# Kernel optimization log

Measured on AMD Instinct MI355X. Metric: run time of the kernel, lower is better.

## Reference

```python
import jax, jax.numpy as jnp
import numpy as np

N = 50000   # nodes
E = 625000  # edges
H = 128     # hidden
B = 32      # bottleneck_dim


def _layernorm(x, g, b, eps=1e-5):
    m = jnp.mean(x, axis=-1, keepdims=True)
    v = jnp.var(x, axis=-1, keepdims=True)
    return (x - m) * jax.lax.rsqrt(v + eps) * g + b


def setup_inputs() -> dict:
    key = jax.random.key(0)
    ks = jax.random.split(key, 16)
    s = 0.05
    return {
        "x": jax.random.normal(ks[0], (N, H), dtype=jnp.float32),
        "edge_index": jax.random.randint(ks[1], (2, E), 0, N, dtype=jnp.int64),
        # down GINConv (eps trainable, init 0) + its bottleneck MLP
        "eps_down": jnp.zeros((), jnp.float32),
        "dw1": jax.random.normal(ks[2], (H, B), dtype=jnp.float32) * s,
        "dg1": jnp.ones((B,), jnp.float32),
        "db1": jnp.zeros((B,), jnp.float32),
        "dw2": jax.random.normal(ks[3], (B, H), dtype=jnp.float32) * s,
        # up GINConv
        "eps_up": jnp.zeros((), jnp.float32),
        "uw1": jax.random.normal(ks[4], (H, B), dtype=jnp.float32) * s,
        "ug1": jnp.ones((B,), jnp.float32),
        "ub1": jnp.zeros((B,), jnp.float32),
        "uw2": jax.random.normal(ks[5], (B, H), dtype=jnp.float32) * s,
        # outer LayerNorms
        "ln1_g": jnp.ones((H,), jnp.float32),
        "ln1_b": jnp.zeros((H,), jnp.float32),
        "ln2_g": jnp.ones((H,), jnp.float32),
        "ln2_b": jnp.zeros((H,), jnp.float32),
        # direction embeddings [2, H]
        "dir_emb": jax.random.normal(ks[6], (2, H), dtype=jnp.float32) * 0.02,
        # combine Linear(2H -> H) with bias
        "cw": jax.random.normal(ks[7], (2 * H, H), dtype=jnp.float32) * s,
        "cb": jnp.zeros((H,), jnp.float32),
    }


def reference(x, edge_index, eps_down, dw1, dg1, db1, dw2,
              eps_up, uw1, ug1, ub1, uw2,
              ln1_g, ln1_b, ln2_g, ln2_b, dir_emb, cw, cb):
    src, dst = edge_index[0], edge_index[1]

    def gin(s_idx, d_idx, eps, w1, g1, b1, w2):
        # scatter-add of source features onto destination nodes
        agg = jax.ops.segment_sum(x[s_idx], d_idx, num_segments=N)  # [N, H]
        h = (1.0 + eps) * x + agg
        # bottleneck MLP: Linear -> LayerNorm -> ReLU -> (Dropout=id) -> Linear
        h = _layernorm(h @ w1, g1, b1)
        return jax.nn.relu(h) @ w2  # [N, H]

    h_down = _layernorm(jax.nn.relu(gin(src, dst, eps_down, dw1, dg1, db1, dw2) + dir_emb[0]), ln1_g, ln1_b)
    # reversed edges for the "up" direction
    h_up = _layernorm(jax.nn.relu(gin(dst, src, eps_up, uw1, ug1, ub1, uw2) + dir_emb[1]), ln2_g, ln2_b)

    h_cat = jnp.concatenate([h_down, h_up], axis=-1)  # [N, 2H]
    return h_cat @ cw + cb  # [N, H]
```

## Files before the change

kernel.cpp:

```cpp
#include <hip/hip_runtime.h>

#define N_NODES 50000
#define NPAD 50048
#define N_EDGES 625000
#define H 128
#define B 32
#define PSTRIDE 40
#define CAP 64
#define NPART 8
#define ROWS_PER_PART (2 * N_NODES / NPART)
#define NGRP 3125
#define YGB 1564
#define CVB 160
#define FILLB (2443 * NPART)

using bf16x8  = __attribute__((ext_vector_type(8))) short;
using f32x4   = __attribute__((ext_vector_type(4))) float;
using u16x4   = __attribute__((ext_vector_type(4))) unsigned short;

static __device__ __forceinline__ unsigned short f2bf(float f) {
    unsigned u = __float_as_uint(f);
    unsigned r = (u + 0x7fff + ((u >> 16) & 1)) >> 16;
    return (unsigned short)r;
}
static __device__ __forceinline__ float bf2f(unsigned short h) {
    return __uint_as_float(((unsigned)h) << 16);
}

__global__ __launch_bounds__(256) void front_kernel(
    const int* __restrict__ ei, int* __restrict__ cursor,
    unsigned short* __restrict__ bucket,
    const float* __restrict__ x,
    const float* __restrict__ dw1, const float* __restrict__ uw1,
    const float* __restrict__ dw2, const float* __restrict__ uw2,
    const float* __restrict__ cw,
    unsigned short* __restrict__ w2h, unsigned short* __restrict__ w2l,
    unsigned short* __restrict__ cwh,
    unsigned short* __restrict__ y)
{
    __shared__ unsigned short wh_lds[32 * 136];
    __shared__ unsigned short wl_lds[32 * 136];

    int b = blockIdx.x;
    if (b < YGB) {
        int dir = (b >= 782) ? 1 : 0;
        int r0b = (b - dir * 782) * 64;
        const float* w1src = dir ? uw1 : dw1;
        for (int j = threadIdx.x; j < 4096; j += 256) {
            int k = j >> 5, c = j & 31;
            float v = w1src[j];
            unsigned short h = f2bf(v);
            wh_lds[c * 136 + k] = h;
            wl_lds[c * 136 + k] = f2bf(v - bf2f(h));
        }
        __syncthreads();

        int w = threadIdx.x >> 6, lane = threadIdx.x & 63;
        int l15 = lane & 15, g = lane >> 4;
        int r0 = r0b + w * 16;
        int node = r0 + l15; if (node >= N_NODES) node = N_NODES - 1;
        const float* xrow = x + (size_t)node * H;

        f32x4 acc[2];
        acc[0] = (f32x4){0.f,0.f,0.f,0.f};
        acc[1] = (f32x4){0.f,0.f,0.f,0.f};
        #pragma unroll
        for (int ks = 0; ks < 4; ++ks) {
            int ko = ks * 32 + g * 8;
            float4 xa = *(const float4*)(xrow + ko);
            float4 xc = *(const float4*)(xrow + ko + 4);
            union { bf16x8 v; unsigned short u[8]; } bb;
            bb.u[0] = f2bf(xa.x); bb.u[1] = f2bf(xa.y);
            bb.u[2] = f2bf(xa.z); bb.u[3] = f2bf(xa.w);
            bb.u[4] = f2bf(xc.x); bb.u[5] = f2bf(xc.y);
            bb.u[6] = f2bf(xc.z); bb.u[7] = f2bf(xc.w);
            #pragma unroll
            for (int t = 0; t < 2; ++t) {
                bf16x8 ah = *(const bf16x8*)(wh_lds + (t * 16 + l15) * 136 + ko);
                bf16x8 al = *(const bf16x8*)(wl_lds + (t * 16 + l15) * 136 + ko);
                acc[t] = __builtin_amdgcn_mfma_f32_16x16x32_bf16(ah, bb.v, acc[t], 0, 0, 0);
                acc[t] = __builtin_amdgcn_mfma_f32_16x16x32_bf16(al, bb.v, acc[t], 0, 0, 0);
            }
        }

        unsigned short* orow = y + ((size_t)dir * NPAD + r0 + l15) * B;
        #pragma unroll
        for (int t = 0; t < 2; ++t) {
            u16x4 o = {f2bf(acc[t][0]), f2bf(acc[t][1]), f2bf(acc[t][2]), f2bf(acc[t][3])};
            *(u16x4*)(orow + t * 16 + g * 4) = o;
        }
        return;
    }
    if (b < YGB + CVB) {
        int i = (b - YGB) * 256 + threadIdx.x;
        if (i < 8192) {
            int j = i & 4095;
            int c = j >> 5, k = j & 31;
            const float* src = (i >> 12) ? uw2 : dw2;
            float v = src[k * 128 + c];
            unsigned short h = f2bf(v);
            w2h[i] = h; w2l[i] = f2bf(v - bf2f(h));
        } else {
            int j = i - 8192;
            int c = j >> 8, k = j & 255;
            cwh[j] = f2bf(cw[k * 128 + c]);
        }
        return;
    }
    int fb = b - (YGB + CVB);
    int p  = fb & 7;
    int eb = fb >> 3;
    int e = eb * 256 + threadIdx.x;
    if (e >= N_EDGES) return;
    int lo = p * ROWS_PER_PART, hi = lo + ROWS_PER_PART;
    int s = ei[e];
    int d = ei[N_EDGES + e];
    int r2 = N_NODES + s;
    if (d >= lo && d < hi) {
        int pos = atomicAdd(&cursor[d], 1);
        if (pos < CAP)
            __builtin_nontemporal_store((unsigned short)s, bucket + (size_t)d * CAP + pos);
    }
    if (r2 >= lo && r2 < hi) {
        int pos = atomicAdd(&cursor[r2], 1);
        if (pos < CAP)
            __builtin_nontemporal_store((unsigned short)d, bucket + (size_t)r2 * CAP + pos);
    }
}

__global__ __launch_bounds__(256) void gather_mlp_kernel(
    const unsigned* __restrict__ y,
    const int* __restrict__ cursor, const unsigned short* __restrict__ bucket,
    const float* __restrict__ eps_d_p, const float* __restrict__ eps_u_p,
    const unsigned short* __restrict__ w2bT_hi, const unsigned short* __restrict__ w2bT_lo,
    const float* __restrict__ dg1, const float* __restrict__ db1,
    const float* __restrict__ ug1, const float* __restrict__ ub1,
    const float* __restrict__ ln1g, const float* __restrict__ ln1b,
    const float* __restrict__ ln2g, const float* __restrict__ ln2b,
    const float* __restrict__ dir_emb,
    unsigned short* __restrict__ hcat)
{
    __shared__ unsigned short plds[4][2][16 * PSTRIDE];

    int w = threadIdx.x >> 6, lane = threadIdx.x & 63;
    int sgrp = lane >> 4, l16 = lane & 15;
    int blk = blockIdx.x;
    int dir = (blk >= 782) ? 1 : 0;
    int r0 = (blk - dir * 782) * 64 + w * 16;

    float eps = 1.f + (dir ? eps_u_p[0] : eps_d_p[0]);
    const unsigned* yu = y + (size_t)dir * NPAD * 16;

    const float* g1p = dir ? ug1 : dg1;
    const float* b1p = dir ? ub1 : db1;
    float2 gv = ((const float2*)g1p)[l16];
    float2 bv = ((const float2*)b1p)[l16];

    unsigned short* mh = &plds[w][0][0];
    unsigned short* ml = &plds[w][1][0];

    for (int p = 0; p < 4; ++p) {
        int rloc = p * 4 + sgrp;
        int node = r0 + rloc;
        float p0 = 0.f, p1 = 0.f;
        if (node < N_NODES) {
            int ridx = dir * N_NODES + node;
            int deg = cursor[ridx]; if (deg > CAP) deg = CAP;
            const unsigned short* nb = bucket + (size_t)ridx * CAP;
            float a0 = 0.f, a1 = 0.f;
            for (int base = 0; base < deg; base += 16) {
                int m = deg - base; if (m > 16) m = 16;
                int id = (l16 < m) ? (int)nb[base + l16] : 0;
                int lim = m - 1;
                for (int j = 0; j < m; j += 8) {
                    unsigned r[8];
                    #pragma unroll
                    for (int q = 0; q < 8; ++q) {
                        int idx = j + q; if (idx > lim) idx = lim;
                        int nbid = __shfl(id, (sgrp << 4) + idx);
                        r[q] = yu[nbid * 16 + l16];
                    }
                    #pragma unroll
                    for (int q = 0; q < 8; ++q) {
                        if (j + q <= lim) {
                            a0 += __uint_as_float(r[q] << 16);
                            a1 += __uint_as_float(r[q] & 0xffff0000u);
                        }
                    }
                }
            }
            unsigned sv = yu[node * 16 + l16];
            float c0 = eps * __uint_as_float(sv << 16) + a0;
            float c1 = eps * __uint_as_float(sv & 0xffff0000u) + a1;
            float ss = c0 + c1, s2 = c0 * c0 + c1 * c1;
            #pragma unroll
            for (int m2 = 1; m2 <= 8; m2 <<= 1) {
                ss += __shfl_xor(ss, m2);
                s2 += __shfl_xor(s2, m2);
            }
            float mean = ss * (1.f / 32.f);
            float var  = s2 * (1.f / 32.f) - mean * mean;
            float rs   = rsqrtf(var + 1e-5f);
            p0 = fmaxf((c0 - mean) * rs * gv.x + bv.x, 0.f);
            p1 = fmaxf((c1 - mean) * rs * gv.y + bv.y, 0.f);
        }
        unsigned short q0 = f2bf(p0), q1 = f2bf(p1);
        *(unsigned*)(mh + rloc * PSTRIDE + 2 * l16) = ((unsigned)q1 << 16) | q0;
        *(unsigned*)(ml + rloc * PSTRIDE + 2 * l16) =
            ((unsigned)f2bf(p1 - bf2f(q1)) << 16) | f2bf(p0 - bf2f(q0));
    }

    int l15 = lane & 15, g = lane >> 4;

    const unsigned short* w2h = w2bT_hi + dir * 4096;
    const unsigned short* w2l = w2bT_lo + dir * 4096;

    bf16x8 pbh = *(const bf16x8*)(mh + l15 * PSTRIDE + g * 8);
    bf16x8 pbl = *(const bf16x8*)(ml + l15 * PSTRIDE + g * 8);

    f32x4 acc2[8];
    #pragma unroll
    for (int t = 0; t < 8; ++t) acc2[t] = (f32x4){0.f,0.f,0.f,0.f};
    #pragma unroll
    for (int t = 0; t < 8; ++t) {
        bf16x8 ah = *(const bf16x8*)(w2h + (t * 16 + l15) * 32 + g * 8);
        bf16x8 al = *(const bf16x8*)(w2l + (t * 16 + l15) * 32 + g * 8);
        acc2[t] = __builtin_amdgcn_mfma_f32_16x16x32_bf16(ah, pbh, acc2[t], 0, 0, 0);
        acc2[t] = __builtin_amdgcn_mfma_f32_16x16x32_bf16(al, pbh, acc2[t], 0, 0, 0);
        acc2[t] = __builtin_amdgcn_mfma_f32_16x16x32_bf16(ah, pbl, acc2[t], 0, 0, 0);
    }

    float av[8][4];
    float u = 0.f, u2 = 0.f;
    #pragma unroll
    for (int t = 0; t < 8; ++t) {
        float4 de = *(const float4*)(dir_emb + dir * H + t * 16 + g * 4);
        av[t][0] = fmaxf(acc2[t][0] + de.x, 0.f);
        av[t][1] = fmaxf(acc2[t][1] + de.y, 0.f);
        av[t][2] = fmaxf(acc2[t][2] + de.z, 0.f);
        av[t][3] = fmaxf(acc2[t][3] + de.w, 0.f);
        #pragma unroll
        for (int r = 0; r < 4; ++r) { u += av[t][r]; u2 += av[t][r] * av[t][r]; }
    }
    u  += __shfl_xor(u, 16);  u  += __shfl_xor(u, 32);
    u2 += __shfl_xor(u2, 16); u2 += __shfl_xor(u2, 32);
    float m2  = u * (1.f / 128.f);
    float v2  = u2 * (1.f / 128.f) - m2 * m2;
    float rs2 = rsqrtf(v2 + 1e-5f);

    const float* lgp = dir ? ln2g : ln1g;
    const float* lbp = dir ? ln2b : ln1b;
    if ((r0 + l15) < N_NODES) {
        unsigned short* orow = hcat + (size_t)(r0 + l15) * 256 + dir * 128;
        #pragma unroll
        for (int t = 0; t < 8; ++t) {
            float4 gg = *(const float4*)(lgp + t * 16 + g * 4);
            float4 bb = *(const float4*)(lbp + t * 16 + g * 4);
            u16x4 o;
            o[0] = f2bf((av[t][0] - m2) * rs2 * gg.x + bb.x);
            o[1] = f2bf((av[t][1] - m2) * rs2 * gg.y + bb.y);
            o[2] = f2bf((av[t][2] - m2) * rs2 * gg.z + bb.z);
            o[3] = f2bf((av[t][3] - m2) * rs2 * gg.w + bb.w);
            *(u16x4*)(orow + t * 16 + g * 4) = o;
        }
    }
}

__global__ __launch_bounds__(256) void combine_mfma(
    const unsigned short* __restrict__ hcat,
    const unsigned short* __restrict__ cwh,
    const float* __restrict__ cb, float* __restrict__ out)
{
    int w = threadIdx.x >> 6, lane = threadIdx.x & 63;
    int l15 = lane & 15, g = lane >> 4;
    int gid = blockIdx.x * 4 + w;
    int q = gid & 3;
    int j = gid >> 2;

    const unsigned short* abase = cwh + (size_t)(q * 32 + l15) * 256 + g * 8;
    bf16x8 Ah[2][8];
    #pragma unroll
    for (int t = 0; t < 2; ++t)
        #pragma unroll
        for (int ks = 0; ks < 8; ++ks)
            Ah[t][ks] = *(const bf16x8*)(abase + (t * 16) * 256 + ks * 32);

    int grp[4]; int ng = 0;
    #pragma unroll
    for (int k = 0; k < 4; ++k) {
        int gg = j + 782 * k;
        if (gg < NGRP) grp[ng++] = gg;
    }
    if (ng == 0) return;

    bf16x8 Bc[8], Bn[8];
    {
        const unsigned short* bb = hcat + (size_t)grp[0] * 16 * 256 + l15 * 256 + g * 8;
        #pragma unroll
        for (int ks = 0; ks < 8; ++ks) Bc[ks] = *(const bf16x8*)(bb + ks * 32);
    }

    float4 bias0 = *(const float4*)(cb + q * 32 + g * 4);
    float4 bias1 = *(const float4*)(cb + q * 32 + 16 + g * 4);

    for (int i = 0; i < ng; ++i) {
        if (i + 1 < ng) {
            const unsigned short* bb = hcat + (size_t)grp[i + 1] * 16 * 256 + l15 * 256 + g * 8;
            #pragma unroll
            for (int ks = 0; ks < 8; ++ks) Bn[ks] = *(const bf16x8*)(bb + ks * 32);
        }

        f32x4 acc0 = (f32x4){0.f,0.f,0.f,0.f};
        f32x4 acc1 = (f32x4){0.f,0.f,0.f,0.f};
        #pragma unroll
        for (int ks = 0; ks < 8; ++ks) {
            acc0 = __builtin_amdgcn_mfma_f32_16x16x32_bf16(Ah[0][ks], Bc[ks], acc0, 0, 0, 0);
            acc1 = __builtin_amdgcn_mfma_f32_16x16x32_bf16(Ah[1][ks], Bc[ks], acc1, 0, 0, 0);
        }

        float* orow = out + (size_t)(grp[i] * 16 + l15) * 128 + q * 32;
        f32x4 v0 = acc0, v1 = acc1;
        v0[0] += bias0.x; v0[1] += bias0.y; v0[2] += bias0.z; v0[3] += bias0.w;
        v1[0] += bias1.x; v1[1] += bias1.y; v1[2] += bias1.z; v1[3] += bias1.w;
        *(f32x4*)(orow + g * 4) = v0;
        *(f32x4*)(orow + 16 + g * 4) = v1;

        #pragma unroll
        for (int ks = 0; ks < 8; ++ks) Bc[ks] = Bn[ks];
    }
}

extern "C" void kernel_launch(void* const* d_in, const int* in_sizes, int n_in,
                              void* d_out, int out_size, void* d_ws, size_t ws_size,
                              hipStream_t stream) {
    const float* x     = (const float*)d_in[0];
    const int*   ei    = (const int*)d_in[1];
    const float* eps_d = (const float*)d_in[2];
    const float* dw1   = (const float*)d_in[3];
    const float* dg1   = (const float*)d_in[4];
    const float* db1   = (const float*)d_in[5];
    const float* dw2   = (const float*)d_in[6];
    const float* eps_u = (const float*)d_in[7];
    const float* uw1   = (const float*)d_in[8];
    const float* ug1   = (const float*)d_in[9];
    const float* ub1   = (const float*)d_in[10];
    const float* uw2   = (const float*)d_in[11];
    const float* ln1g  = (const float*)d_in[12];
    const float* ln1b  = (const float*)d_in[13];
    const float* ln2g  = (const float*)d_in[14];
    const float* ln2b  = (const float*)d_in[15];
    const float* dire  = (const float*)d_in[16];
    const float* cw    = (const float*)d_in[17];
    const float* cb    = (const float*)d_in[18];

    int* cursor = (int*)d_ws;
    unsigned short* bucket = (unsigned short*)(cursor + 2 * N_NODES);
    unsigned short* yarr = bucket + (size_t)2 * N_NODES * CAP;
    unsigned short* hcat = yarr + (size_t)2 * NPAD * B;
    unsigned short* w2bT_hi = hcat + (size_t)N_NODES * 256;
    unsigned short* w2bT_lo = w2bT_hi + 8192;
    unsigned short* cwbT_hi = w2bT_lo + 8192;

    hipMemsetAsync(cursor, 0, 2 * N_NODES * sizeof(int), stream);

    front_kernel<<<YGB + CVB + FILLB, 256, 0, stream>>>(
        ei, cursor, bucket, x, dw1, uw1, dw2, uw2, cw,
        w2bT_hi, w2bT_lo, cwbT_hi, yarr);

    gather_mlp_kernel<<<1564, 256, 0, stream>>>(
        (const unsigned*)yarr, cursor, bucket, eps_d, eps_u,
        w2bT_hi, w2bT_lo,
        dg1, db1, ug1, ub1, ln1g, ln1b, ln2g, ln2b, dire, hcat);

    combine_mfma<<<782, 256, 0, stream>>>(hcat, cwbT_hi, cb, (float*)d_out);
}
```

Baseline: 145.8 us.

## Replace per-partition edge fill with two-pass LDS binning and staged scatter

The old edge fill read the edge list once per partition, launching eight blocks per edge chunk. Each block appended to a partition's bucket only when the destination fell inside it. Now each block reads its edges once and bins packed (row, neighbour) entries by partition in LDS. It flushes each bin to a contiguous per-partition staging region with one global atomic per bin. A new scatter kernel then walks each partition's staging region and does the per-row atomic bucket inserts, so the atomics are localized per partition. This cuts redundant edge reads but adds a kernel launch and a round trip through a roughly 5.9 MB staging buffer.

```diff
diff --git a/kernel.cpp b/kernel.cpp
--- a/kernel.cpp
+++ b/kernel.cpp
@@ -12,7 +12,10 @@
 #define NGRP 3125
 #define YGB 1564
 #define CVB 160
-#define FILLB (2443 * NPART)
+#define EPB 1024
+#define BINB ((N_EDGES + EPB - 1) / EPB)
+#define NS 512
+#define SLOT 184320
 
 using bf16x8  = __attribute__((ext_vector_type(8))) short;
 using f32x4   = __attribute__((ext_vector_type(4))) float;
@@ -28,8 +31,9 @@
 }
 
 __global__ __launch_bounds__(256) void front_kernel(
-    const int* __restrict__ ei, int* __restrict__ cursor,
-    unsigned short* __restrict__ bucket,
+    const int* __restrict__ ei, int* __restrict__ bin_cursor,
+    int* __restrict__ cursor, unsigned short* __restrict__ bucket,
+    unsigned* __restrict__ staging,
     const float* __restrict__ x,
     const float* __restrict__ dw1, const float* __restrict__ uw1,
     const float* __restrict__ dw2, const float* __restrict__ uw2,
@@ -38,8 +42,10 @@
     unsigned short* __restrict__ cwh,
     unsigned short* __restrict__ y)
 {
-    __shared__ unsigned short wh_lds[32 * 136];
-    __shared__ unsigned short wl_lds[32 * 136];
+    __shared__ union {
+        struct { unsigned short wh[32 * 136], wl[32 * 136]; } yg;
+        struct { unsigned bins[NPART][NS]; int bcnt[NPART]; } bn;
+    } sm;
 
     int b = blockIdx.x;
     if (b < YGB) {
@@ -50,8 +56,8 @@
             int k = j >> 5, c = j & 31;
             float v = w1src[j];
             unsigned short h = f2bf(v);
-            wh_lds[c * 136 + k] = h;
-            wl_lds[c * 136 + k] = f2bf(v - bf2f(h));
+            sm.yg.wh[c * 136 + k] = h;
+            sm.yg.wl[c * 136 + k] = f2bf(v - bf2f(h));
         }
         __syncthreads();
 
@@ -76,8 +82,8 @@
             bb.u[6] = f2bf(xc.z); bb.u[7] = f2bf(xc.w);
             #pragma unroll
             for (int t = 0; t < 2; ++t) {
-                bf16x8 ah = *(const bf16x8*)(wh_lds + (t * 16 + l15) * 136 + ko);
-                bf16x8 al = *(const bf16x8*)(wl_lds + (t * 16 + l15) * 136 + ko);
+                bf16x8 ah = *(const bf16x8*)(sm.yg.wh + (t * 16 + l15) * 136 + ko);
+                bf16x8 al = *(const bf16x8*)(sm.yg.wl + (t * 16 + l15) * 136 + ko);
                 acc[t] = __builtin_amdgcn_mfma_f32_16x16x32_bf16(ah, bb.v, acc[t], 0, 0, 0);
                 acc[t] = __builtin_amdgcn_mfma_f32_16x16x32_bf16(al, bb.v, acc[t], 0, 0, 0);
             }
@@ -107,24 +113,73 @@
         }
         return;
     }
+    if (threadIdx.x < NPART) sm.bn.bcnt[threadIdx.x] = 0;
+    __syncthreads();
+
     int fb = b - (YGB + CVB);
-    int p  = fb & 7;
-    int eb = fb >> 3;
-    int e = eb * 256 + threadIdx.x;
-    if (e >= N_EDGES) return;
-    int lo = p * ROWS_PER_PART, hi = lo + ROWS_PER_PART;
-    int s = ei[e];
-    int d = ei[N_EDGES + e];
-    int r2 = N_NODES + s;
-    if (d >= lo && d < hi) {
-        int pos = atomicAdd(&cursor[d], 1);
-        if (pos < CAP)
-            __builtin_nontemporal_store((unsigned short)s, bucket + (size_t)d * CAP + pos);
-    }
-    if (r2 >= lo && r2 < hi) {
-        int pos = atomicAdd(&cursor[r2], 1);
-        if (pos < CAP)
-            __builtin_nontemporal_store((unsigned short)d, bucket + (size_t)r2 * CAP + pos);
+    int e0 = fb * EPB;
+    int elim = e0 + EPB; if (elim > N_EDGES) elim = N_EDGES;
+    for (int e = e0 + threadIdx.x; e < elim; e += 256) {
+        int s = ei[e];
+        int d = ei[N_EDGES + e];
+        {
+            int p1 = d / ROWS_PER_PART;
+            unsigned ent = ((unsigned)(d - p1 * ROWS_PER_PART) << 16) | (unsigned)s;
+            int pos = atomicAdd(&sm.bn.bcnt[p1], 1);
+            if (pos < NS) sm.bn.bins[p1][pos] = ent;
+            else {
+                int pp = atomicAdd(&cursor[d], 1);
+                if (pp < CAP) bucket[(size_t)d * CAP + pp] = (unsigned short)s;
+            }
+        }
+        {
+            int r2 = N_NODES + s;
+            int p2 = r2 / ROWS_PER_PART;
+            unsigned ent = ((unsigned)(r2 - p2 * ROWS_PER_PART) << 16) | (unsigned)d;
+            int pos = atomicAdd(&sm.bn.bcnt[p2], 1);
+            if (pos < NS) sm.bn.bins[p2][pos] = ent;
+            else {
+                int pp = atomicAdd(&cursor[r2], 1);
+                if (pp < CAP) bucket[(size_t)r2 * CAP + pp] = (unsigned short)d;
+            }
+        }
+    }
+    __syncthreads();
+
+    int w = threadIdx.x >> 6, lane = threadIdx.x & 63;
+    for (int bb = w; bb < NPART; bb += 4) {
+        int cnt = sm.bn.bcnt[bb]; if (cnt > NS) cnt = NS;
+        int base = 0;
+        if (lane == 0) base = atomicAdd(&bin_cursor[bb], cnt);
+        base = __shfl(base, 0);
+        for (int i = lane; i < cnt; i += 64) {
+            unsigned ent = sm.bn.bins[bb][i];
+            int gpos = base + i;
+            if (gpos < SLOT) {
+                staging[(size_t)bb * SLOT + gpos] = ent;
+            } else {
+                int row = bb * ROWS_PER_PART + (int)(ent >> 16);
+                int pp = atomicAdd(&cursor[row], 1);
+                if (pp < CAP) bucket[(size_t)row * CAP + pp] = (unsigned short)(ent & 0xffffu);
+            }
+        }
+    }
+}
+
+__global__ __launch_bounds__(256) void scatter_kernel(
+    const unsigned* __restrict__ staging, const int* __restrict__ bin_cursor,
+    int* __restrict__ cursor, unsigned short* __restrict__ bucket)
+{
+    int p = blockIdx.x & 7;
+    int cnt = bin_cursor[p]; if (cnt > SLOT) cnt = SLOT;
+    int idx = (blockIdx.x >> 3) * 256 + threadIdx.x;
+    int stride = (gridDim.x >> 3) * 256;
+    const unsigned* st = staging + (size_t)p * SLOT;
+    for (int i = idx; i < cnt; i += stride) {
+        unsigned ent = st[i];
+        int row = p * ROWS_PER_PART + (int)(ent >> 16);
+        int pos = atomicAdd(&cursor[row], 1);
+        if (pos < CAP) bucket[(size_t)row * CAP + pos] = (unsigned short)(ent & 0xffffu);
     }
 }
 
@@ -353,19 +408,24 @@
     const float* cw    = (const float*)d_in[17];
     const float* cb    = (const float*)d_in[18];
 
-    int* cursor = (int*)d_ws;
+    int* bin_cursor = (int*)d_ws;
+    int* cursor = bin_cursor + 16;
     unsigned short* bucket = (unsigned short*)(cursor + 2 * N_NODES);
-    unsigned short* yarr = bucket + (size_t)2 * N_NODES * CAP;
+    unsigned* staging = (unsigned*)(bucket + (size_t)2 * N_NODES * CAP);
+    unsigned short* yarr = (unsigned short*)(staging + (size_t)NPART * SLOT);
     unsigned short* hcat = yarr + (size_t)2 * NPAD * B;
     unsigned short* w2bT_hi = hcat + (size_t)N_NODES * 256;
     unsigned short* w2bT_lo = w2bT_hi + 8192;
     unsigned short* cwbT_hi = w2bT_lo + 8192;
 
-    hipMemsetAsync(cursor, 0, 2 * N_NODES * sizeof(int), stream);
-
-    front_kernel<<<YGB + CVB + FILLB, 256, 0, stream>>>(
-        ei, cursor, bucket, x, dw1, uw1, dw2, uw2, cw,
+    hipMemsetAsync(d_ws, 0, (16 + 2 * N_NODES) * sizeof(int), stream);
+
+    front_kernel<<<YGB + CVB + BINB, 256, 0, stream>>>(
+        ei, bin_cursor, cursor, bucket, staging,
+        x, dw1, uw1, dw2, uw2, cw,
         w2bT_hi, w2bT_lo, cwbT_hi, yarr);
+
+    scatter_kernel<<<1024, 256, 0, stream>>>(staging, bin_cursor, cursor, bucket);
 
     gather_mlp_kernel<<<1564, 256, 0, stream>>>(
         (const unsigned*)yarr, cursor, bucket, eps_d, eps_u,
```

Result: slower. 194.0 us (+33.1%).

## Replace global-atomic bucket fill with wave-binned staging and LDS bucket build

Applied to the files above, without the earlier changes.

The adjacency bucket fill no longer uses global atomics on per-node cursors across eight partition passes over the edges. Each wave now sorts its edges into eight partition stripes in a staging buffer using ballot/popcount prefix offsets, and sends rare overflows to a small global list. A new build kernel then gives each block a row range of one partition, builds that range's buckets with LDS atomics, and writes cursors and buckets out contiguously, which also removes the large cursor memset. The cost is an extra kernel launch, and every build block rescans its whole partition stripe (including empty slots). The overflow list is also walked serially by a single thread.

```diff
diff --git a/kernel.cpp b/kernel.cpp
--- a/kernel.cpp
+++ b/kernel.cpp
@@ -12,7 +12,13 @@
 #define NGRP 3125
 #define YGB 1564
 #define CVB 160
-#define FILLB (2443 * NPART)
+#define BINB 611
+#define NWAVES (BINB * 4)
+#define WCH 128
+#define PSTRIPE (NWAVES * WCH)
+#define OVFMAX 1024
+#define RPB 496
+#define SUBB 26
 
 using bf16x8  = __attribute__((ext_vector_type(8))) short;
 using f32x4   = __attribute__((ext_vector_type(4))) float;
@@ -28,8 +34,9 @@
 }
 
 __global__ __launch_bounds__(256) void front_kernel(
-    const int* __restrict__ ei, int* __restrict__ cursor,
-    unsigned short* __restrict__ bucket,
+    const int* __restrict__ ei,
+    int* __restrict__ ovf_cnt, unsigned long long* __restrict__ ovf,
+    int* __restrict__ wcnt, unsigned* __restrict__ staging,
     const float* __restrict__ x,
     const float* __restrict__ dw1, const float* __restrict__ uw1,
     const float* __restrict__ dw2, const float* __restrict__ uw2,
@@ -108,23 +115,115 @@
         return;
     }
     int fb = b - (YGB + CVB);
-    int p  = fb & 7;
-    int eb = fb >> 3;
-    int e = eb * 256 + threadIdx.x;
-    if (e >= N_EDGES) return;
-    int lo = p * ROWS_PER_PART, hi = lo + ROWS_PER_PART;
-    int s = ei[e];
-    int d = ei[N_EDGES + e];
-    int r2 = N_NODES + s;
-    if (d >= lo && d < hi) {
-        int pos = atomicAdd(&cursor[d], 1);
-        if (pos < CAP)
-            __builtin_nontemporal_store((unsigned short)s, bucket + (size_t)d * CAP + pos);
-    }
-    if (r2 >= lo && r2 < hi) {
-        int pos = atomicAdd(&cursor[r2], 1);
-        if (pos < CAP)
-            __builtin_nontemporal_store((unsigned short)d, bucket + (size_t)r2 * CAP + pos);
+    int w = threadIdx.x >> 6, lane = threadIdx.x & 63;
+    int gwave = fb * 4 + w;
+    unsigned long long lmask = (lane == 63) ? 0x7fffffffffffffffull
+                                            : ((1ull << lane) - 1ull);
+    unsigned sbase = (unsigned)gwave * WCH;
+    int cnt[8] = {0,0,0,0,0,0,0,0};
+
+    for (int r = 0; r < 4; ++r) {
+        int e = fb * 1024 + w * 256 + r * 64 + lane;
+        bool valid = e < N_EDGES;
+        int s = valid ? ei[e] : 0;
+        int d = valid ? ei[N_EDGES + e] : 0;
+        int p1 = (unsigned)d / ROWS_PER_PART;
+        unsigned ent1 = ((unsigned)(d - p1 * ROWS_PER_PART) << 16) | (unsigned)s;
+        int r2 = N_NODES + s;
+        int p2 = (unsigned)r2 / ROWS_PER_PART;
+        unsigned ent2 = ((unsigned)(r2 - p2 * ROWS_PER_PART) << 16) | (unsigned)d;
+
+        #pragma unroll
+        for (int p = 0; p < 4; ++p) {
+            unsigned long long m = __ballot(valid && (p1 == p));
+            if (valid && p1 == p) {
+                int pos = cnt[p] + __popcll(m & lmask);
+                if (pos < WCH)
+                    staging[(size_t)p * PSTRIPE + sbase + pos] = ent1;
+                else {
+                    int op = atomicAdd(ovf_cnt, 1);
+                    if (op < OVFMAX)
+                        ovf[op] = ((unsigned long long)p << 32) | (unsigned long long)ent1;
+                }
+            }
+            cnt[p] += __popcll(m);
+        }
+        #pragma unroll
+        for (int p = 4; p < 8; ++p) {
+            unsigned long long m = __ballot(valid && (p2 == p));
+            if (valid && p2 == p) {
+                int pos = cnt[p] + __popcll(m & lmask);
+                if (pos < WCH)
+                    staging[(size_t)p * PSTRIPE + sbase + pos] = ent2;
+                else {
+                    int op = atomicAdd(ovf_cnt, 1);
+                    if (op < OVFMAX)
+                        ovf[op] = ((unsigned long long)p << 32) | (unsigned long long)ent2;
+                }
+            }
+            cnt[p] += __popcll(m);
+        }
+    }
+    #pragma unroll
+    for (int p = 0; p < 8; ++p)
+        if (lane == p) wcnt[gwave * 8 + p] = cnt[p];
+}
+
+__global__ __launch_bounds__(256) void build_kernel(
+    const unsigned* __restrict__ staging, const int* __restrict__ wcnt,
+    const int* __restrict__ ovf_cnt, const unsigned long long* __restrict__ ovf,
+    int* __restrict__ cursor, unsigned short* __restrict__ bucket)
+{
+    __shared__ unsigned short lbkt[RPB * CAP];
+    __shared__ int lcnt[RPB];
+
+    int p   = blockIdx.x & 7;
+    int sub = blockIdx.x >> 3;
+    int rlo = sub * RPB;
+    int nrows = ROWS_PER_PART - rlo; if (nrows > RPB) nrows = RPB;
+
+    for (int i = threadIdx.x; i < RPB; i += 256) lcnt[i] = 0;
+    __syncthreads();
+
+    const unsigned* st = staging + (size_t)p * PSTRIPE;
+    int half = threadIdx.x >> 7;
+    int i128 = threadIdx.x & 127;
+    for (int it = 0; it < NWAVES / 2; ++it) {
+        int c = it * 2 + half;
+        unsigned ent = st[(size_t)c * WCH + i128];
+        int cnt = wcnt[c * 8 + p];
+        if (i128 < cnt) {
+            int row = (int)(ent >> 16) - rlo;
+            if (row >= 0 && row < RPB) {
+                int lp = atomicAdd(&lcnt[row], 1);
+                if (lp < CAP) lbkt[row * CAP + lp] = (unsigned short)(ent & 0xffffu);
+            }
+        }
+    }
+    if (threadIdx.x == 0) {
+        int oc = ovf_cnt[0]; if (oc > OVFMAX) oc = OVFMAX;
+        for (int i = 0; i < oc; ++i) {
+            unsigned long long e = ovf[i];
+            if ((int)(e >> 32) == p) {
+                int row = (int)((e >> 16) & 0xffffu) - rlo;
+                if (row >= 0 && row < RPB) {
+                    int lp = atomicAdd(&lcnt[row], 1);
+                    if (lp < CAP) lbkt[row * CAP + lp] = (unsigned short)(e & 0xffffu);
+                }
+            }
+        }
+    }
+    __syncthreads();
+
+    int growbase = p * ROWS_PER_PART + rlo;
+    for (int r = threadIdx.x; r < nrows; r += 256) {
+        int c = lcnt[r]; if (c > CAP) c = CAP;
+        cursor[growbase + r] = c;
+    }
+    for (int i = threadIdx.x; i < nrows * 32; i += 256) {
+        int r = i >> 5, dw = i & 31;
+        ((unsigned*)(bucket + (size_t)(growbase + r) * CAP))[dw] =
+            ((const unsigned*)(lbkt + r * CAP))[dw];
     }
 }
 
@@ -353,19 +452,27 @@
     const float* cw    = (const float*)d_in[17];
     const float* cb    = (const float*)d_in[18];
 
-    int* cursor = (int*)d_ws;
+    int* ovf_cnt = (int*)d_ws;
+    unsigned long long* ovf = (unsigned long long*)(ovf_cnt + 16);
+    int* wcnt = (int*)(ovf + OVFMAX);
+    int* cursor = wcnt + NWAVES * 8;
     unsigned short* bucket = (unsigned short*)(cursor + 2 * N_NODES);
-    unsigned short* yarr = bucket + (size_t)2 * N_NODES * CAP;
+    unsigned* staging = (unsigned*)(bucket + (size_t)2 * N_NODES * CAP);
+    unsigned short* yarr = (unsigned short*)(staging + (size_t)NPART * PSTRIPE);
     unsigned short* hcat = yarr + (size_t)2 * NPAD * B;
     unsigned short* w2bT_hi = hcat + (size_t)N_NODES * 256;
     unsigned short* w2bT_lo = w2bT_hi + 8192;
     unsigned short* cwbT_hi = w2bT_lo + 8192;
 
-    hipMemsetAsync(cursor, 0, 2 * N_NODES * sizeof(int), stream);
-
-    front_kernel<<<YGB + CVB + FILLB, 256, 0, stream>>>(
-        ei, cursor, bucket, x, dw1, uw1, dw2, uw2, cw,
+    hipMemsetAsync(ovf_cnt, 0, 16 * sizeof(int), stream);
+
+    front_kernel<<<YGB + CVB + BINB, 256, 0, stream>>>(
+        ei, ovf_cnt, ovf, wcnt, staging,
+        x, dw1, uw1, dw2, uw2, cw,
         w2bT_hi, w2bT_lo, cwbT_hi, yarr);
+
+    build_kernel<<<NPART * SUBB, 256, 0, stream>>>(
+        staging, wcnt, ovf_cnt, ovf, cursor, bucket);
 
     gather_mlp_kernel<<<1564, 256, 0, stream>>>(
         (const unsigned*)yarr, cursor, bucket, eps_d, eps_u,
```

New measurement: 555.3 us. +281.0%, slower.
